# Kernel optimization log

Hardware: AMD Instinct MI355X
Metric: run time of the kernel (lower is better)

## Reference

```python
import jax, jax.numpy as jnp
import numpy as np

EMBED_DIM = 1024
NUM_HEADS = 16
HEAD_DIM = EMBED_DIM // NUM_HEADS  # 64
SCALING = 0.125
T, B = 2048, 2


def setup_inputs() -> dict:
    key = jax.random.key(0)
    k_q, k_len, k_w1, k_b1, k_w2, k_b2 = jax.random.split(key, 6)
    query = jax.random.normal(k_q, (T, B, EMBED_DIM), dtype=jnp.float32)
    # realistic padding: each sequence has a valid length in [T//2, T)
    lengths = jax.random.randint(k_len, (B,), T // 2, T)
    key_padding_mask = jnp.arange(T)[None, :] >= lengths[:, None]  # [B, T] bool, True = pad
    s1 = 1.0 / np.sqrt(EMBED_DIM)
    W_in = jax.random.uniform(k_w1, (3 * EMBED_DIM, EMBED_DIM), jnp.float32, -s1, s1)
    b_in = jax.random.uniform(k_b1, (3 * EMBED_DIM,), jnp.float32, -s1, s1)
    W_out = jax.random.uniform(k_w2, (EMBED_DIM, EMBED_DIM), jnp.float32, -s1, s1)
    b_out = jax.random.uniform(k_b2, (EMBED_DIM,), jnp.float32, -s1, s1)
    return {"query": query, "key_padding_mask": key_padding_mask,
            "W_in": W_in, "b_in": b_in, "W_out": W_out, "b_out": b_out}


def reference(query, key_padding_mask, W_in, b_in, W_out, b_out):
    # query: [T, B, E]; key_padding_mask: [B, S] bool (True = padded key)
    t, b, e = query.shape
    h, hd = NUM_HEADS, HEAD_DIM
    proj = query @ W_in.T + b_in                      # [T, B, 3E]
    q, k, v = jnp.split(proj, 3, axis=-1)             # each [T, B, E]
    q = q * SCALING

    def to_bh(x):  # [T, B, E] -> [B*H, T, hd], matching torch view+transpose
        return x.reshape(t, b * h, hd).transpose(1, 0, 2)

    q, k, v = to_bh(q), to_bh(k), to_bh(v)
    attn_weights = jnp.einsum('bth,bsh->bts', q, k)   # [B*H, T, S]
    attn_weights = attn_weights.reshape(b, h, t, t)
    attn_weights = jnp.where(key_padding_mask[:, None, None, :], -jnp.inf, attn_weights)
    # softmax computed in float32 then cast back, as in the original
    attn_weights = jax.nn.softmax(attn_weights.astype(jnp.float32), axis=-1).astype(query.dtype)
    # dropout p=0 (eval/inference) -> identity
    attn = jnp.einsum('bhts,bhsd->bhtd', attn_weights, v.reshape(b, h, t, hd))  # [B,H,T,hd]
    attn = attn.reshape(b * h, t, hd).transpose(1, 0, 2).reshape(t, b, e)       # [T,B,E]
    return attn @ W_out.T + b_out
```

## Files before the change

### kernel.cpp

```cpp
#include <hip/hip_runtime.h>
#include <hip/hip_bf16.h>
#include <stdint.h>
#include <stddef.h>

typedef __hip_bfloat16 bf16;
typedef __attribute__((ext_vector_type(4))) float f32x4;
typedef __attribute__((ext_vector_type(8))) short s16x8;
typedef __attribute__((ext_vector_type(4))) short s16x4;

#define AS1 __attribute__((address_space(1)))
#define AS3 __attribute__((address_space(3)))

__device__ __forceinline__ void async_ld16(const void* g, void* l) {
  __builtin_amdgcn_global_load_lds((AS1 void*)g, (AS3 void*)l, 16, 0, 0);
}

#if __has_builtin(__builtin_amdgcn_exp2f)
#define EXP2F(x) __builtin_amdgcn_exp2f(x)
#else
#define EXP2F(x) exp2f(x)
#endif

__device__ __forceinline__ unsigned pk_bf16(float a, float b) {
  unsigned ua = __builtin_bit_cast(unsigned, a);
  unsigned ub = __builtin_bit_cast(unsigned, b);
  ua += 0x7FFFu + ((ua >> 16) & 1u);
  ub += 0x7FFFu + ((ub >> 16) & 1u);
  return (ua >> 16) | (ub & 0xFFFF0000u);
}

__device__ __forceinline__ unsigned pk_trunc(float a, float b) {
  return __builtin_amdgcn_perm(__builtin_bit_cast(unsigned, b),
                               __builtin_bit_cast(unsigned, a), 0x07060302u);
}

__global__ __launch_bounds__(256) void convert_all_kernel(const float* __restrict__ q_src,
                                                          const float* __restrict__ wi_src,
                                                          const float* __restrict__ wo_src,
                                                          bf16* __restrict__ q_dst,
                                                          bf16* __restrict__ wi_dst,
                                                          bf16* __restrict__ wo_dst,
                                                          const void* __restrict__ mask,
                                                          int* __restrict__ lengths) {
  int blk = blockIdx.x;
  if (blk >= 4096) {
    __shared__ int s_any;
    __shared__ int s_cnt[256];
    const int tid = threadIdx.x;
    const int b = blk - 4096;
    const unsigned char* m8 = (const unsigned char*)mask;
    if (tid == 0) s_any = 0;
    __syncthreads();
    int local = 0;
    for (int i = tid; i < 4096; i += 256) local |= m8[i];
    if (local) atomicOr(&s_any, 1);
    __syncthreads();
    int cnt = 0;
    if (s_any) {
      for (int t = tid; t < 2048; t += 256) cnt += (m8[b * 2048 + t] == 0) ? 1 : 0;
    } else {
      const int* m32 = (const int*)mask;
      for (int t = tid; t < 2048; t += 256) cnt += (m32[b * 2048 + t] == 0) ? 1 : 0;
    }
    s_cnt[tid] = cnt;
    __syncthreads();
    for (int s = 128; s > 0; s >>= 1) {
      if (tid < s) s_cnt[tid] += s_cnt[tid + s];
      __syncthreads();
    }
    if (tid == 0) lengths[b] = s_cnt[0];
    return;
  }
  const float* src;
  bf16* dst;
  int base;
  if (blk < 2048)      { src = q_src;  dst = q_dst;  base = blk * 2048; }
  else if (blk < 3584) { src = wi_src; dst = wi_dst; base = (blk - 2048) * 2048; }
  else                 { src = wo_src; dst = wo_dst; base = (blk - 3584) * 2048; }
  int i = base + threadIdx.x * 8;
  float4 a = *(const float4*)(src + i);
  float4 b = *(const float4*)(src + i + 4);
  unsigned u[4];
  u[0] = pk_bf16(a.x, a.y); u[1] = pk_bf16(a.z, a.w);
  u[2] = pk_bf16(b.x, b.y); u[3] = pk_bf16(b.z, b.w);
  *(uint4*)(dst + i) = *(const uint4*)u;
}

__device__ __forceinline__ void gemm_mainloop(const bf16* __restrict__ A,
                                              const bf16* __restrict__ Bm,
                                              bf16* As, bf16* Bs,
                                              int m0, int n0, f32x4 (&acc)[4][4]) {
  const int K = 1024;
  const int tid = threadIdx.x;
  const int wave = tid >> 6, lane = tid & 63;
  const int col = lane & 15, quad = lane >> 4;
  const int wm = wave & 1, wn = wave >> 1;
#pragma unroll
  for (int mi = 0; mi < 4; mi++)
#pragma unroll
    for (int ni = 0; ni < 4; ni++) acc[mi][ni] = (f32x4){0.f, 0.f, 0.f, 0.f};

  const int c0 = wave * 128 + lane;
  const int rowA0 = c0 >> 2, kc0 = (c0 & 3) * 8;
  const int c1 = c0 + 64;
  const int rowA1 = c1 >> 2, kc1 = (c1 & 3) * 8;
  char* ldsA0 = (char*)As + (size_t)(wave * 128) * 16;
  char* ldsA1 = ldsA0 + 64 * 16;
  char* ldsB0 = (char*)Bs + (size_t)(wave * 128) * 16;
  char* ldsB1 = ldsB0 + 64 * 16;
  const bf16* gA0 = A + (size_t)(m0 + rowA0) * K + kc0;
  const bf16* gA1 = A + (size_t)(m0 + rowA1) * K + kc1;
  const bf16* gB0 = Bm + (size_t)(n0 + rowA0) * K + kc0;
  const bf16* gB1 = Bm + (size_t)(n0 + rowA1) * K + kc1;

  for (int k0 = 0; k0 < K; k0 += 32) {
    async_ld16(gA0 + k0, ldsA0);
    async_ld16(gA1 + k0, ldsA1);
    async_ld16(gB0 + k0, ldsB0);
    async_ld16(gB1 + k0, ldsB1);
    __syncthreads();
    s16x8 af[4], bfr[4];
#pragma unroll
    for (int mi = 0; mi < 4; mi++)
      af[mi] = *(const s16x8*)(As + (wm * 64 + mi * 16 + col) * 32 + quad * 8);
#pragma unroll
    for (int ni = 0; ni < 4; ni++)
      bfr[ni] = *(const s16x8*)(Bs + (wn * 64 + ni * 16 + col) * 32 + quad * 8);
#pragma unroll
    for (int mi = 0; mi < 4; mi++)
#pragma unroll
      for (int ni = 0; ni < 4; ni++)
        acc[mi][ni] = __builtin_amdgcn_mfma_f32_16x16x32_bf16(af[mi], bfr[ni], acc[mi][ni], 0, 0, 0);
    __syncthreads();
  }
}

__global__ __launch_bounds__(256) void gemm_qkv(const bf16* __restrict__ X,
                                                const bf16* __restrict__ W,
                                                const float* __restrict__ bias,
                                                bf16* __restrict__ Qd,
                                                bf16* __restrict__ Kd,
                                                bf16* __restrict__ Vt) {
  __shared__ bf16 As[128 * 32];
  __shared__ bf16 Bs[128 * 32];
  const int m0 = blockIdx.y * 128, n0 = blockIdx.x * 128;
  f32x4 acc[4][4];
  gemm_mainloop(X, W, As, Bs, m0, n0, acc);
  const int tid = threadIdx.x;
  const int wave = tid >> 6, lane = tid & 63;
  const int col = lane & 15, quad = lane >> 4;
  const int wm = wave & 1, wn = wave >> 1;
  const float QSCALE = 0.125f * 1.4426950408889634f;
#pragma unroll
  for (int mi = 0; mi < 4; mi++)
#pragma unroll
    for (int ni = 0; ni < 4; ni++)
#pragma unroll
      for (int r = 0; r < 4; r++) {
        int m = m0 + wm * 64 + mi * 16 + quad * 4 + r;
        int n = n0 + wn * 64 + ni * 16 + col;
        float v = acc[mi][ni][r] + bias[n];
        int e = n & 1023, hh = e >> 6, d = e & 63;
        int t = m >> 1, b = m & 1;
        int bh = b * 16 + hh;
        if (n < 1024) {
          Qd[((size_t)bh * 2048 + t) * 64 + d] = __float2bfloat16(v * QSCALE);
        } else if (n < 2048) {
          Kd[((size_t)bh * 2048 + t) * 64 + d] = __float2bfloat16(v);
        } else {
          int sl = t & 63;
          int perm = ((sl >> 2) & 3) * 16 + (sl >> 4) * 4 + (sl & 3);
          Vt[(size_t)bh * 131072 + (t >> 6) * 4096 + d * 64 + perm] = __float2bfloat16(v);
        }
      }
}

__global__ __launch_bounds__(256, 4) void attn_kernel(const bf16* __restrict__ Qd,
                                                      const bf16* __restrict__ Kd,
                                                      const bf16* __restrict__ Vt,
                                                      const int* __restrict__ lengths,
                                                      bf16* __restrict__ attn_out) {
  __shared__ bf16 Ks[2][64 * 64];
  __shared__ bf16 Vs[2][64 * 64];

  const int bh = blockIdx.y;
  const int b = bh >> 4, h = bh & 15;
  const int qt0 = blockIdx.x * 64;
  const int tid = threadIdx.x;
  const int wave = tid >> 6, lane = tid & 63;
  const int col = lane & 15, quad = lane >> 4;
  const int len = lengths[b];
  const int nfull = len >> 6;
  const int rem = len & 63;
  const int nkt = nfull + (rem ? 1 : 0);

  const bf16* qptr = Qd + ((size_t)bh * 2048 + qt0 + wave * 16 + col) * 64 + quad * 8;
  const s16x8 bq0 = *(const s16x8*)(qptr);
  const s16x8 bq1 = *(const s16x8*)(qptr + 32);

  const int kbase0 = col * 128 + ((quad ^ (col & 7)) << 4);
  const int kbase1 = kbase0 ^ 64;
  const int vbase0 = col * 128 + (((quad << 1) ^ (col & 7)) << 4);
  const int vbase1 = vbase0 ^ 16;

  const bf16* Kg = Kd + (size_t)bh * 2048 * 64;
  const bf16* Vg = Vt + (size_t)bh * 131072;
  const int c0 = wave * 128 + lane, c1 = c0 + 64;
  const int r0 = c0 >> 3, j0 = (c0 & 7) ^ (r0 & 7);
  const int r1 = c1 >> 3, j1 = (c1 & 7) ^ (r1 & 7);
  const bf16* gK0 = Kg + r0 * 64 + j0 * 8;
  const bf16* gK1 = Kg + r1 * 64 + j1 * 8;
  const bf16* gV0 = Vg + r0 * 64 + j0 * 8;
  const bf16* gV1 = Vg + r1 * 64 + j1 * 8;
  const int dst0 = (wave * 128) * 16, dst1 = (wave * 128 + 64) * 16;

  auto stage = [&](int kt, int BUF) {
    const int off = kt * 4096;
    async_ld16(gK0 + off, (char*)Ks + BUF + dst0);
    async_ld16(gK1 + off, (char*)Ks + BUF + dst1);
    async_ld16(gV0 + off, (char*)Vs + BUF + dst0);
    async_ld16(gV1 + off, (char*)Vs + BUF + dst1);
  };

  const s16x4 aOnes = {0x3F80, 0x3F80, 0x3F80, 0x3F80};
  const f32x4 Zf = (f32x4){0.f, 0.f, 0.f, 0.f};
  f32x4 lacc = Zf;
  f32x4 oaccT[4];
#pragma unroll
  for (int dt = 0; dt < 4; dt++) oaccT[dt] = Zf;

  auto score = [&](int BUF, f32x4 (&sacc)[4]) {
#pragma unroll
    for (int ti = 0; ti < 4; ti++) {
      const s16x8 ak0 = *(const s16x8*)((char*)Ks + BUF + ti * 2048 + kbase0);
      sacc[ti] = __builtin_amdgcn_mfma_f32_16x16x32_bf16(ak0, bq0, Zf, 0, 0, 0);
      const s16x8 ak1 = *(const s16x8*)((char*)Ks + BUF + ti * 2048 + kbase1);
      sacc[ti] = __builtin_amdgcn_mfma_f32_16x16x32_bf16(ak1, bq1, sacc[ti], 0, 0, 0);
    }
  };
  auto accum = [&](int BUF, s16x4 (&bP)[4]) {
#pragma unroll
    for (int ti = 0; ti < 4; ti++)
      lacc = __builtin_amdgcn_mfma_f32_16x16x16bf16_1k(aOnes, bP[ti], lacc, 0, 0, 0);
#pragma unroll
    for (int dt = 0; dt < 4; dt++) {
#pragma unroll
      for (int sh = 0; sh < 2; sh++) {
        const s16x8 av = *(const s16x8*)((char*)Vs + BUF + dt * 2048 + (sh ? vbase1 : vbase0));
        const s16x4 alo = __builtin_shufflevector(av, av, 0, 1, 2, 3);
        const s16x4 ahi = __builtin_shufflevector(av, av, 4, 5, 6, 7);
        oaccT[dt] = __builtin_amdgcn_mfma_f32_16x16x16bf16_1k(alo, bP[sh * 2], oaccT[dt], 0, 0, 0);
        oaccT[dt] = __builtin_amdgcn_mfma_f32_16x16x16bf16_1k(ahi, bP[sh * 2 + 1], oaccT[dt], 0, 0, 0);
      }
    }
  };

  auto tile_full = [&](int BUF) {
    f32x4 sacc[4];
    score(BUF, sacc);
    s16x4 bP[4];
#pragma unroll
    for (int ti = 0; ti < 4; ti++) {
      uint2 u = {pk_trunc(EXP2F(sacc[ti][0]), EXP2F(sacc[ti][1])),
                 pk_trunc(EXP2F(sacc[ti][2]), EXP2F(sacc[ti][3]))};
      bP[ti] = __builtin_bit_cast(s16x4, u);
    }
    accum(BUF, bP);
  };

  auto tile_mask = [&](int BUF) {
    f32x4 sacc[4];
    score(BUF, sacc);
    s16x4 bP[4];
#pragma unroll
    for (int ti = 0; ti < 4; ti++) {
      const int sb = ti * 16 + quad * 4;
      float p0 = (sb + 0 < rem) ? EXP2F(sacc[ti][0]) : 0.f;
      float p1 = (sb + 1 < rem) ? EXP2F(sacc[ti][1]) : 0.f;
      float p2 = (sb + 2 < rem) ? EXP2F(sacc[ti][2]) : 0.f;
      float p3 = (sb + 3 < rem) ? EXP2F(sacc[ti][3]) : 0.f;
      uint2 u = {pk_trunc(p0, p1), pk_trunc(p2, p3)};
      bP[ti] = __builtin_bit_cast(s16x4, u);
    }
    accum(BUF, bP);
  };

  stage(0, 0);
  __syncthreads();
  int kt = 0;
  for (;;) {
    if (kt + 1 < nkt) stage(kt + 1, 8192);
    if (kt < nfull) tile_full(0); else tile_mask(0);
    __syncthreads();
    if (++kt >= nkt) break;
    if (kt + 1 < nkt) stage(kt + 1, 0);
    if (kt < nfull) tile_full(8192); else tile_mask(8192);
    __syncthreads();
    if (++kt >= nkt) break;
  }

  const float linv = 1.0f / lacc[0];
  const int t = qt0 + wave * 16 + col;
  bf16* outp = attn_out + ((size_t)t * 2 + b) * 1024 + h * 64 + quad * 4;
#pragma unroll
  for (int dt = 0; dt < 4; dt++) {
    uint2 u = {pk_bf16(oaccT[dt][0] * linv, oaccT[dt][1] * linv),
               pk_bf16(oaccT[dt][2] * linv, oaccT[dt][3] * linv)};
    *(uint2*)(outp + dt * 16) = u;
  }
}

__global__ __launch_bounds__(256) void gemm_out(const bf16* __restrict__ Aa,
                                                const bf16* __restrict__ W,
                                                const float* __restrict__ bias,
                                                float* __restrict__ out) {
  __shared__ bf16 Bs[128 * 32];
  __shared__ bf16 As[64 * 32];
  const int K = 1024;
  const int m0 = blockIdx.y * 64, n0 = blockIdx.x * 128;
  const int tid = threadIdx.x;
  const int wave = tid >> 6, lane = tid & 63;
  const int col = lane & 15, quad = lane >> 4;

  f32x4 acc[8];
#pragma unroll
  for (int ni = 0; ni < 8; ni++) acc[ni] = (f32x4){0.f, 0.f, 0.f, 0.f};

  const int cB0 = wave * 64 + lane, cB1 = cB0 + 256;
  const int rB0 = cB0 >> 2, kB0 = (cB0 & 3) * 8;
  const int rB1 = cB1 >> 2, kB1 = (cB1 & 3) * 8;
  const bf16* gB0 = W + (size_t)(n0 + rB0) * K + kB0;
  const bf16* gB1 = W + (size_t)(n0 + rB1) * K + kB1;
  char* ldsB0 = (char*)Bs + (size_t)(wave * 64) * 16;
  char* ldsB1 = (char*)Bs + (size_t)(256 + wave * 64) * 16;
  const int rA = cB0 >> 2, kA = (cB0 & 3) * 8;
  const bf16* gA = Aa + (size_t)(m0 + rA) * K + kA;
  char* ldsA = (char*)As + (size_t)(wave * 64) * 16;

  for (int k0 = 0; k0 < K; k0 += 32) {
    async_ld16(gB0 + k0, ldsB0);
    async_ld16(gB1 + k0, ldsB1);
    async_ld16(gA + k0, ldsA);
    __syncthreads();
    const s16x8 af = *(const s16x8*)(As + (wave * 16 + col) * 32 + quad * 8);
#pragma unroll
    for (int ni = 0; ni < 8; ni++) {
      const s16x8 bfr = *(const s16x8*)(Bs + (ni * 16 + col) * 32 + quad * 8);
      acc[ni] = __builtin_amdgcn_mfma_f32_16x16x32_bf16(af, bfr, acc[ni], 0, 0, 0);
    }
    __syncthreads();
  }

#pragma unroll
  for (int ni = 0; ni < 8; ni++)
#pragma unroll
    for (int r = 0; r < 4; r++) {
      int m = m0 + wave * 16 + quad * 4 + r;
      int n = n0 + ni * 16 + col;
      out[(size_t)m * 1024 + n] = acc[ni][r] + bias[n];
    }
}

extern "C" void kernel_launch(void* const* d_in, const int* in_sizes, int n_in,
                              void* d_out, int out_size, void* d_ws, size_t ws_size,
                              hipStream_t stream) {
  (void)in_sizes; (void)n_in; (void)out_size; (void)ws_size;
  const float* query = (const float*)d_in[0];
  const void*  mask  = d_in[1];
  const float* W_in  = (const float*)d_in[2];
  const float* b_in  = (const float*)d_in[3];
  const float* W_out = (const float*)d_in[4];
  const float* b_out = (const float*)d_in[5];
  float* out = (float*)d_out;

  char* ws = (char*)d_ws;
  bf16* Xbf    = (bf16*)(ws);
  bf16* attnb  = (bf16*)(ws);
  bf16* Winbf  = (bf16*)(ws + 8388608);
  bf16* Woutbf = (bf16*)(ws + 8388608 + 6291456);
  bf16* Qd     = (bf16*)(ws + 16777216);
  bf16* Kd     = (bf16*)(ws + 25165824);
  bf16* Vt     = (bf16*)(ws + 33554432);
  int*  lens   = (int*)(ws + 41943040);

  convert_all_kernel<<<4098, 256, 0, stream>>>(query, W_in, W_out, Xbf, Winbf, Woutbf,
                                               mask, lens);
  gemm_qkv<<<dim3(24, 32), 256, 0, stream>>>(Xbf, Winbf, b_in, Qd, Kd, Vt);
  attn_kernel<<<dim3(32, 32), 256, 0, stream>>>(Qd, Kd, Vt, lens, attnb);
  gemm_out<<<dim3(8, 64), 256, 0, stream>>>(attnb, Woutbf, b_out, out);
}
```

Baseline: 198.2 us.

## Double query rows per attention block and deepen K step in output GEMM

The attention kernel now processes 128 query rows per block (two 16-row groups per wave), so each K/V tile staged in LDS is reused across twice as many queries. This halves the grid and global K/V traffic at the cost of more registers, hence launch bounds drop to 2 blocks per SIMD. Separately, the output GEMM loads a K-depth of 64 per iteration instead of 32, halving the number of barrier-separated loop steps while doubling LDS use. With only 512 attention blocks, fewer waves may be resident across the CUs.

```diff
diff --git a/kernel.cpp b/kernel.cpp
--- a/kernel.cpp
+++ b/kernel.cpp
@@ -175,7 +175,7 @@
       }
 }
 
-__global__ __launch_bounds__(256, 4) void attn_kernel(const bf16* __restrict__ Qd,
+__global__ __launch_bounds__(256, 2) void attn_kernel(const bf16* __restrict__ Qd,
                                                       const bf16* __restrict__ Kd,
                                                       const bf16* __restrict__ Vt,
                                                       const int* __restrict__ lengths,
@@ -185,7 +185,7 @@
 
   const int bh = blockIdx.y;
   const int b = bh >> 4, h = bh & 15;
-  const int qt0 = blockIdx.x * 64;
+  const int qt0 = blockIdx.x * 128;
   const int tid = threadIdx.x;
   const int wave = tid >> 6, lane = tid & 63;
   const int col = lane & 15, quad = lane >> 4;
@@ -194,9 +194,14 @@
   const int rem = len & 63;
   const int nkt = nfull + (rem ? 1 : 0);
 
-  const bf16* qptr = Qd + ((size_t)bh * 2048 + qt0 + wave * 16 + col) * 64 + quad * 8;
-  const s16x8 bq0 = *(const s16x8*)(qptr);
-  const s16x8 bq1 = *(const s16x8*)(qptr + 32);
+  s16x8 bq[2][2];
+#pragma unroll
+  for (int g = 0; g < 2; g++) {
+    const bf16* qptr =
+        Qd + ((size_t)bh * 2048 + qt0 + wave * 32 + g * 16 + col) * 64 + quad * 8;
+    bq[g][0] = *(const s16x8*)(qptr);
+    bq[g][1] = *(const s16x8*)(qptr + 32);
+  }
 
   const int kbase0 = col * 128 + ((quad ^ (col & 7)) << 4);
   const int kbase1 = kbase0 ^ 64;
@@ -224,24 +229,30 @@
 
   const s16x4 aOnes = {0x3F80, 0x3F80, 0x3F80, 0x3F80};
   const f32x4 Zf = (f32x4){0.f, 0.f, 0.f, 0.f};
-  f32x4 lacc = Zf;
-  f32x4 oaccT[4];
-#pragma unroll
-  for (int dt = 0; dt < 4; dt++) oaccT[dt] = Zf;
-
-  auto score = [&](int BUF, f32x4 (&sacc)[4]) {
+  f32x4 lacc[2] = {Zf, Zf};
+  f32x4 oaccT[2][4];
+#pragma unroll
+  for (int g = 0; g < 2; g++)
+#pragma unroll
+    for (int dt = 0; dt < 4; dt++) oaccT[g][dt] = Zf;
+
+  auto score = [&](int BUF, f32x4 (&s0)[4], f32x4 (&s1)[4]) {
 #pragma unroll
     for (int ti = 0; ti < 4; ti++) {
       const s16x8 ak0 = *(const s16x8*)((char*)Ks + BUF + ti * 2048 + kbase0);
-      sacc[ti] = __builtin_amdgcn_mfma_f32_16x16x32_bf16(ak0, bq0, Zf, 0, 0, 0);
+      s0[ti] = __builtin_amdgcn_mfma_f32_16x16x32_bf16(ak0, bq[0][0], Zf, 0, 0, 0);
+      s1[ti] = __builtin_amdgcn_mfma_f32_16x16x32_bf16(ak0, bq[1][0], Zf, 0, 0, 0);
       const s16x8 ak1 = *(const s16x8*)((char*)Ks + BUF + ti * 2048 + kbase1);
-      sacc[ti] = __builtin_amdgcn_mfma_f32_16x16x32_bf16(ak1, bq1, sacc[ti], 0, 0, 0);
+      s0[ti] = __builtin_amdgcn_mfma_f32_16x16x32_bf16(ak1, bq[0][1], s0[ti], 0, 0, 0);
+      s1[ti] = __builtin_amdgcn_mfma_f32_16x16x32_bf16(ak1, bq[1][1], s1[ti], 0, 0, 0);
     }
   };
-  auto accum = [&](int BUF, s16x4 (&bP)[4]) {
-#pragma unroll
-    for (int ti = 0; ti < 4; ti++)
-      lacc = __builtin_amdgcn_mfma_f32_16x16x16bf16_1k(aOnes, bP[ti], lacc, 0, 0, 0);
+  auto accum = [&](int BUF, s16x4 (&bP0)[4], s16x4 (&bP1)[4]) {
+#pragma unroll
+    for (int ti = 0; ti < 4; ti++) {
+      lacc[0] = __builtin_amdgcn_mfma_f32_16x16x16bf16_1k(aOnes, bP0[ti], lacc[0], 0, 0, 0);
+      lacc[1] = __builtin_amdgcn_mfma_f32_16x16x16bf16_1k(aOnes, bP1[ti], lacc[1], 0, 0, 0);
+    }
 #pragma unroll
     for (int dt = 0; dt < 4; dt++) {
 #pragma unroll
@@ -249,40 +260,51 @@
         const s16x8 av = *(const s16x8*)((char*)Vs + BUF + dt * 2048 + (sh ? vbase1 : vbase0));
         const s16x4 alo = __builtin_shufflevector(av, av, 0, 1, 2, 3);
         const s16x4 ahi = __builtin_shufflevector(av, av, 4, 5, 6, 7);
-        oaccT[dt] = __builtin_amdgcn_mfma_f32_16x16x16bf16_1k(alo, bP[sh * 2], oaccT[dt], 0, 0, 0);
-        oaccT[dt] = __builtin_amdgcn_mfma_f32_16x16x16bf16_1k(ahi, bP[sh * 2 + 1], oaccT[dt], 0, 0, 0);
+        oaccT[0][dt] = __builtin_amdgcn_mfma_f32_16x16x16bf16_1k(alo, bP0[sh * 2], oaccT[0][dt], 0, 0, 0);
+        oaccT[0][dt] = __builtin_amdgcn_mfma_f32_16x16x16bf16_1k(ahi, bP0[sh * 2 + 1], oaccT[0][dt], 0, 0, 0);
+        oaccT[1][dt] = __builtin_amdgcn_mfma_f32_16x16x16bf16_1k(alo, bP1[sh * 2], oaccT[1][dt], 0, 0, 0);
+        oaccT[1][dt] = __builtin_amdgcn_mfma_f32_16x16x16bf16_1k(ahi, bP1[sh * 2 + 1], oaccT[1][dt], 0, 0, 0);
       }
     }
   };
 
   auto tile_full = [&](int BUF) {
-    f32x4 sacc[4];
-    score(BUF, sacc);
-    s16x4 bP[4];
+    f32x4 s0[4], s1[4];
+    score(BUF, s0, s1);
+    s16x4 bP0[4], bP1[4];
 #pragma unroll
     for (int ti = 0; ti < 4; ti++) {
-      uint2 u = {pk_trunc(EXP2F(sacc[ti][0]), EXP2F(sacc[ti][1])),
-                 pk_trunc(EXP2F(sacc[ti][2]), EXP2F(sacc[ti][3]))};
-      bP[ti] = __builtin_bit_cast(s16x4, u);
-    }
-    accum(BUF, bP);
+      uint2 u0 = {pk_trunc(EXP2F(s0[ti][0]), EXP2F(s0[ti][1])),
+                  pk_trunc(EXP2F(s0[ti][2]), EXP2F(s0[ti][3]))};
+      bP0[ti] = __builtin_bit_cast(s16x4, u0);
+      uint2 u1 = {pk_trunc(EXP2F(s1[ti][0]), EXP2F(s1[ti][1])),
+                  pk_trunc(EXP2F(s1[ti][2]), EXP2F(s1[ti][3]))};
+      bP1[ti] = __builtin_bit_cast(s16x4, u1);
+    }
+    accum(BUF, bP0, bP1);
   };
 
   auto tile_mask = [&](int BUF) {
-    f32x4 sacc[4];
-    score(BUF, sacc);
-    s16x4 bP[4];
+    f32x4 s0[4], s1[4];
+    score(BUF, s0, s1);
+    s16x4 bP0[4], bP1[4];
 #pragma unroll
     for (int ti = 0; ti < 4; ti++) {
       const int sb = ti * 16 + quad * 4;
-      float p0 = (sb + 0 < rem) ? EXP2F(sacc[ti][0]) : 0.f;
-      float p1 = (sb + 1 < rem) ? EXP2F(sacc[ti][1]) : 0.f;
-      float p2 = (sb + 2 < rem) ? EXP2F(sacc[ti][2]) : 0.f;
-      float p3 = (sb + 3 < rem) ? EXP2F(sacc[ti][3]) : 0.f;
-      uint2 u = {pk_trunc(p0, p1), pk_trunc(p2, p3)};
-      bP[ti] = __builtin_bit_cast(s16x4, u);
-    }
-    accum(BUF, bP);
+      float a0 = (sb + 0 < rem) ? EXP2F(s0[ti][0]) : 0.f;
+      float a1 = (sb + 1 < rem) ? EXP2F(s0[ti][1]) : 0.f;
+      float a2 = (sb + 2 < rem) ? EXP2F(s0[ti][2]) : 0.f;
+      float a3 = (sb + 3 < rem) ? EXP2F(s0[ti][3]) : 0.f;
+      uint2 u0 = {pk_trunc(a0, a1), pk_trunc(a2, a3)};
+      bP0[ti] = __builtin_bit_cast(s16x4, u0);
+      float c0m = (sb + 0 < rem) ? EXP2F(s1[ti][0]) : 0.f;
+      float c1m = (sb + 1 < rem) ? EXP2F(s1[ti][1]) : 0.f;
+      float c2m = (sb + 2 < rem) ? EXP2F(s1[ti][2]) : 0.f;
+      float c3m = (sb + 3 < rem) ? EXP2F(s1[ti][3]) : 0.f;
+      uint2 u1 = {pk_trunc(c0m, c1m), pk_trunc(c2m, c3m)};
+      bP1[ti] = __builtin_bit_cast(s16x4, u1);
+    }
+    accum(BUF, bP0, bP1);
   };
 
   stage(0, 0);
@@ -299,14 +321,17 @@
     if (++kt >= nkt) break;
   }
 
-  const float linv = 1.0f / lacc[0];
-  const int t = qt0 + wave * 16 + col;
-  bf16* outp = attn_out + ((size_t)t * 2 + b) * 1024 + h * 64 + quad * 4;
-#pragma unroll
-  for (int dt = 0; dt < 4; dt++) {
-    uint2 u = {pk_bf16(oaccT[dt][0] * linv, oaccT[dt][1] * linv),
-               pk_bf16(oaccT[dt][2] * linv, oaccT[dt][3] * linv)};
-    *(uint2*)(outp + dt * 16) = u;
+#pragma unroll
+  for (int g = 0; g < 2; g++) {
+    const float linv = 1.0f / lacc[g][0];
+    const int t = qt0 + wave * 32 + g * 16 + col;
+    bf16* outp = attn_out + ((size_t)t * 2 + b) * 1024 + h * 64 + quad * 4;
+#pragma unroll
+    for (int dt = 0; dt < 4; dt++) {
+      uint2 u = {pk_bf16(oaccT[g][dt][0] * linv, oaccT[g][dt][1] * linv),
+                 pk_bf16(oaccT[g][dt][2] * linv, oaccT[g][dt][3] * linv)};
+      *(uint2*)(outp + dt * 16) = u;
+    }
   }
 }
 
@@ -314,8 +339,8 @@
                                                 const bf16* __restrict__ W,
                                                 const float* __restrict__ bias,
                                                 float* __restrict__ out) {
-  __shared__ bf16 Bs[128 * 32];
-  __shared__ bf16 As[64 * 32];
+  __shared__ bf16 Bs[128 * 64];
+  __shared__ bf16 As[64 * 64];
   const int K = 1024;
   const int m0 = blockIdx.y * 64, n0 = blockIdx.x * 128;
   const int tid = threadIdx.x;
@@ -326,27 +351,37 @@
 #pragma unroll
   for (int ni = 0; ni < 8; ni++) acc[ni] = (f32x4){0.f, 0.f, 0.f, 0.f};
 
-  const int cB0 = wave * 64 + lane, cB1 = cB0 + 256;
-  const int rB0 = cB0 >> 2, kB0 = (cB0 & 3) * 8;
-  const int rB1 = cB1 >> 2, kB1 = (cB1 & 3) * 8;
-  const bf16* gB0 = W + (size_t)(n0 + rB0) * K + kB0;
-  const bf16* gB1 = W + (size_t)(n0 + rB1) * K + kB1;
-  char* ldsB0 = (char*)Bs + (size_t)(wave * 64) * 16;
-  char* ldsB1 = (char*)Bs + (size_t)(256 + wave * 64) * 16;
-  const int rA = cB0 >> 2, kA = (cB0 & 3) * 8;
-  const bf16* gA = Aa + (size_t)(m0 + rA) * K + kA;
-  char* ldsA = (char*)As + (size_t)(wave * 64) * 16;
-
-  for (int k0 = 0; k0 < K; k0 += 32) {
-    async_ld16(gB0 + k0, ldsB0);
-    async_ld16(gB1 + k0, ldsB1);
-    async_ld16(gA + k0, ldsA);
-    __syncthreads();
-    const s16x8 af = *(const s16x8*)(As + (wave * 16 + col) * 32 + quad * 8);
+  const bf16* gB[4];
+  char* ldsB[4];
+#pragma unroll
+  for (int i = 0; i < 4; i++) {
+    const int c = tid + 256 * i;
+    gB[i] = W + (size_t)(n0 + (c >> 3)) * K + (c & 7) * 8;
+    ldsB[i] = (char*)Bs + (size_t)(wave * 64 + 256 * i) * 16;
+  }
+  const bf16* gA[2];
+  char* ldsA[2];
+#pragma unroll
+  for (int i = 0; i < 2; i++) {
+    const int c = tid + 256 * i;
+    gA[i] = Aa + (size_t)(m0 + (c >> 3)) * K + (c & 7) * 8;
+    ldsA[i] = (char*)As + (size_t)(wave * 64 + 256 * i) * 16;
+  }
+
+  for (int k0 = 0; k0 < K; k0 += 64) {
+#pragma unroll
+    for (int i = 0; i < 4; i++) async_ld16(gB[i] + k0, ldsB[i]);
+#pragma unroll
+    for (int i = 0; i < 2; i++) async_ld16(gA[i] + k0, ldsA[i]);
+    __syncthreads();
+    const s16x8 af0 = *(const s16x8*)(As + (wave * 16 + col) * 64 + quad * 8);
+    const s16x8 af1 = *(const s16x8*)(As + (wave * 16 + col) * 64 + 32 + quad * 8);
 #pragma unroll
     for (int ni = 0; ni < 8; ni++) {
-      const s16x8 bfr = *(const s16x8*)(Bs + (ni * 16 + col) * 32 + quad * 8);
-      acc[ni] = __builtin_amdgcn_mfma_f32_16x16x32_bf16(af, bfr, acc[ni], 0, 0, 0);
+      const s16x8 b0 = *(const s16x8*)(Bs + (ni * 16 + col) * 64 + quad * 8);
+      acc[ni] = __builtin_amdgcn_mfma_f32_16x16x32_bf16(af0, b0, acc[ni], 0, 0, 0);
+      const s16x8 b1 = *(const s16x8*)(Bs + (ni * 16 + col) * 64 + 32 + quad * 8);
+      acc[ni] = __builtin_amdgcn_mfma_f32_16x16x32_bf16(af1, b1, acc[ni], 0, 0, 0);
     }
     __syncthreads();
   }
@@ -386,6 +421,6 @@
   convert_all_kernel<<<4098, 256, 0, stream>>>(query, W_in, W_out, Xbf, Winbf, Woutbf,
                                                mask, lens);
   gemm_qkv<<<dim3(24, 32), 256, 0, stream>>>(Xbf, Winbf, b_in, Qd, Kd, Vt);
-  attn_kernel<<<dim3(32, 32), 256, 0, stream>>>(Qd, Kd, Vt, lens, attnb);
+  attn_kernel<<<dim3(16, 32), 256, 0, stream>>>(Qd, Kd, Vt, lens, attnb);
   gemm_out<<<dim3(8, 64), 256, 0, stream>>>(attnb, Woutbf, b_out, out);
 }
```

Measured after the change: 198.0 us. About the same (-0.1%).
